# Kernel optimization log

Hardware: AMD Instinct MI355X
Metric: run time of the kernel (lower is better)

Reference implementation:

```python
import jax, jax.numpy as jnp
import numpy as np

N_HEADS = 16


def setup_inputs() -> dict:
    key = jax.random.key(0)
    k1, k2, k3 = jax.random.split(key, 3)
    B, S, D = 2, 2048, 1024
    x = jax.random.normal(k1, (B, S, D), dtype=jnp.float32)
    # causal mask: 1 = keep, 0 = masked (module does masked_fill(mask == 0, -inf))
    mask = jnp.broadcast_to(jnp.tril(jnp.ones((S, S), dtype=jnp.int32)), (B, S, S))
    # torch Linear(bias=False) weights, stored transposed so y = x @ W
    w_qkv = jax.random.normal(k2, (D, 3 * D), dtype=jnp.float32) * (1.0 / np.sqrt(D))
    w_out = jax.random.normal(k3, (D, D), dtype=jnp.float32) * (1.0 / np.sqrt(D))
    return {"x": x, "mask": mask, "w_qkv": w_qkv, "w_out": w_out}


def reference(x, mask, w_qkv, w_out):
    B, S, D = x.shape
    H = N_HEADS
    dh = D // H
    scale = 1.0 / np.sqrt(dh)

    qkv = x @ w_qkv                                   # [B,S,3D]
    qkv = qkv.reshape(B, S, 3, H, dh)
    qkv = jnp.transpose(qkv, (2, 0, 3, 1, 4))         # [3,B,H,S,dh]
    q, k, v = qkv[0], qkv[1], qkv[2]

    scores = jnp.einsum("bhqd,bhkd->bhqk", q, k) * scale   # [B,H,S,S]
    scores = jnp.where(mask[:, None, :, :] == 0, -jnp.inf, scores)
    attn = jax.nn.softmax(scores, axis=-1)            # dropout = identity (eval)

    out = jnp.einsum("bhqk,bhkd->bhqd", attn, v)      # [B,H,S,dh]
    out = jnp.transpose(out, (0, 2, 1, 3)).reshape(B, S, D)
    return out @ w_out
```

## Files before the change

kernel.cpp:

```cpp
#include <hip/hip_runtime.h>

typedef unsigned short u16;
typedef unsigned int u32;
typedef u16 u16x8 __attribute__((ext_vector_type(8)));
typedef u16 u16x4 __attribute__((ext_vector_type(4)));
typedef u32 u32x4 __attribute__((ext_vector_type(4)));
typedef __bf16 bf16x8 __attribute__((ext_vector_type(8)));
typedef float f32x4 __attribute__((ext_vector_type(4)));
typedef float f32x16 __attribute__((ext_vector_type(16)));


static __device__ __forceinline__ u16 bf16_rn(float f) {
    union { float f; u32 u; } a; a.f = f;
    u32 u = a.u;
    return (u16)((u + 0x7FFFu + ((u >> 16) & 1u)) >> 16);
}

static __device__ __forceinline__ bf16x8 as_bf(u16x8 v) {
    return __builtin_bit_cast(bf16x8, v);
}

static __device__ __forceinline__ u32 cvt_pk_bf16(float lo, float hi) {
    u32 r;
    asm("v_cvt_pk_bf16_f32 %0, %1, %2" : "=v"(r) : "v"(lo), "v"(hi));
    return r;
}

static __device__ __forceinline__ void glds16(const u16* g, u16* lds) {
    __builtin_amdgcn_global_load_lds(
        (const __attribute__((address_space(1))) void*)g,
        (__attribute__((address_space(3))) void*)lds, 16, 0, 0);
}


__global__ void k_prep(const float* __restrict__ x, u16* __restrict__ xb,
                       const float* __restrict__ w_qkv, u16* __restrict__ wqkvT,
                       const float* __restrict__ w_out, u16* __restrict__ woutT) {
    __shared__ float t[32][33];
    const int bid = blockIdx.x, tid = threadIdx.x;
    if (bid < 2048) {
        const int i = bid * 256 + tid;
        const float4* s = (const float4*)x + (size_t)i * 2;
        float4 a = s[0], b = s[1];
        u16x8 v;
        v[0] = bf16_rn(a.x); v[1] = bf16_rn(a.y); v[2] = bf16_rn(a.z); v[3] = bf16_rn(a.w);
        v[4] = bf16_rn(b.x); v[5] = bf16_rn(b.y); v[6] = bf16_rn(b.z); v[7] = bf16_rn(b.w);
        *(u16x8*)(xb + (size_t)i * 8) = v;
        return;
    }
    const float* src; u16* dst; int R, C, bxi, byi;
    if (bid < 5120) {
        const int tb = bid - 2048;
        src = w_qkv; dst = wqkvT; R = 1024; C = 3072;
        bxi = tb % 96; byi = tb / 96;
    } else {
        const int tb = bid - 5120;
        src = w_out; dst = woutT; R = 1024; C = 1024;
        bxi = tb % 32; byi = tb / 32;
    }
    const int tx = tid & 31, ty = tid >> 5;
    const int bx = bxi * 32, by = byi * 32;
#pragma unroll
    for (int j = 0; j < 32; j += 8)
        t[ty + j][tx] = src[(size_t)(by + ty + j) * C + bx + tx];
    __syncthreads();
#pragma unroll
    for (int j = 0; j < 32; j += 8)
        dst[(size_t)(bx + ty + j) * R + by + tx] = bf16_rn(t[tx][ty + j]);
}


template <int MODE>
__launch_bounds__(256, 2)
__global__ void k_gemm(const u16* __restrict__ A, const u16* __restrict__ Bt,
                       void* __restrict__ outp, int M, int N, int K) {
    __shared__ __align__(16) u16 As[2][128 * 32];
    __shared__ __align__(16) u16 Bs[2][128 * 32];
    const int tid = threadIdx.x;
    const int l = tid & 63, wv = tid >> 6;
    const int wr = wv >> 1, wc = wv & 1;
    const int l15 = l & 15, lg = l >> 4;
    const int m0 = blockIdx.y * 128, n0 = blockIdx.x * 128;
    const int NT = K >> 5;

    const f32x4 fzero = {0.f, 0.f, 0.f, 0.f};
    f32x4 acc[4][4];
#pragma unroll
    for (int m = 0; m < 4; m++)
#pragma unroll
        for (int n = 0; n < 4; n++) acc[m][n] = fzero;

    const int grow0 = wv * 32 + (l >> 2);
    const int gcol = (l & 3) * 8;

    auto stage = [&](int buf, int kt) {
        const size_t ko = (size_t)kt * 32 + gcol;
        glds16(A  + (size_t)(m0 + grow0) * K + ko,      &As[buf][wv * 1024]);
        glds16(A  + (size_t)(m0 + grow0 + 16) * K + ko, &As[buf][wv * 1024 + 512]);
        glds16(Bt + (size_t)(n0 + grow0) * K + ko,      &Bs[buf][wv * 1024]);
        glds16(Bt + (size_t)(n0 + grow0 + 16) * K + ko, &Bs[buf][wv * 1024 + 512]);
    };

    stage(0, 0);
    int cur = 0;
    for (int kt = 0; kt < NT; ++kt) {
        if (kt + 1 < NT) {
            stage(cur ^ 1, kt + 1);
            asm volatile("s_waitcnt vmcnt(4)" ::: "memory");
        } else {
            asm volatile("s_waitcnt vmcnt(0)" ::: "memory");
        }
        __builtin_amdgcn_s_barrier();
        u16x8 af[4], bfv[4];
#pragma unroll
        for (int m = 0; m < 4; m++)
            af[m] = *(const u16x8*)(&As[cur][(wr * 64 + m * 16 + l15) * 32 + lg * 8]);
#pragma unroll
        for (int n = 0; n < 4; n++)
            bfv[n] = *(const u16x8*)(&Bs[cur][(wc * 64 + n * 16 + l15) * 32 + lg * 8]);
#pragma unroll
        for (int m = 0; m < 4; m++)
#pragma unroll
            for (int n = 0; n < 4; n++)
                acc[m][n] = __builtin_amdgcn_mfma_f32_16x16x32_bf16(
                    as_bf(af[m]), as_bf(bfv[n]), acc[m][n], 0, 0, 0);
        __builtin_amdgcn_s_barrier();
        cur ^= 1;
    }

    if (MODE == 0) {
        u16* qkv = (u16*)outp;
#pragma unroll
        for (int m = 0; m < 4; m++) {
            const int rb = m0 + wr * 64 + m * 16 + lg * 4;
#pragma unroll
            for (int n = 0; n < 4; n++) {
                const int c = n0 + wc * 64 + n * 16;
                const int t = c >> 10, h = (c >> 6) & 15, d0 = (c & 63) + l15;
                const float scl = (t == 0) ? 0.18033688011112042f : 1.0f;
#pragma unroll
                for (int i = 0; i < 4; i++) {
                    const int r = rb + i;
                    const int b = r >> 11, s = r & 2047;
                    qkv[((((size_t)t * 2 + b) * 16 + h) * 2048 + s) * 64 + d0] =
                        bf16_rn(acc[m][n][i] * scl);
                }
            }
        }
    } else {
        float* O = (float*)outp;
#pragma unroll
        for (int m = 0; m < 4; m++) {
            const int rb = m0 + wr * 64 + m * 16 + lg * 4;
#pragma unroll
            for (int n = 0; n < 4; n++) {
                const int c = n0 + wc * 64 + n * 16 + l15;
#pragma unroll
                for (int i = 0; i < 4; i++)
                    O[(size_t)(rb + i) * N + c] = acc[m][n][i];
            }
        }
    }
}


__launch_bounds__(256, 2)
__global__ void k_attn(const u16* __restrict__ qkv, u16* __restrict__ ab) {
    __shared__ __align__(16) char arena[4][9216];
    __shared__ float MLs[4][64];
    const int tid = threadIdx.x, l = tid & 63, wv = tid >> 6;
    const int q = l & 31, h = l >> 5;
    const int bid = blockIdx.x;
    const int bh = bid & 31;
    const int pp = bid >> 5;
    const int b = bh >> 4, hd = bh & 15;
    const size_t plane = (size_t)2048 * 64;
    const u16* Qg = qkv + ((size_t)(0 + b) * 16 + hd) * plane;
    const u16* Kg = qkv + ((size_t)(2 + b) * 16 + hd) * plane;
    const u16* Vg = qkv + ((size_t)(4 + b) * 16 + hd) * plane;
    u16* VT = (u16*)arena[wv];

    const int g = l & 7, qd = l >> 3;
    const u16* Kbase = Kg + (size_t)q * 64 + 8 * h;
    const u16* Vbase = Vg + (size_t)(8 * qd) * 64 + 8 * g;
    const int Fq0 = 8 * (q >> 3) + ((q & 7) ^ ((q >> 3) & 7));
    const int d1 = q + 32;
    const int Fq1 = 8 * (d1 >> 3) + ((d1 & 7) ^ ((d1 >> 3) & 7));
    const u16* vr0 = VT + Fq0 * 72 + 8 * h;
    const u16* vr1 = VT + Fq1 * 72 + 8 * h;
    const float FIXM = 12.0f;

    for (int ph = 0; ph < 2; ++ph) {
        const int qt = ph ? 63 - pp : pp;
        const int q0 = qt * 32, qg = q0 + q;
        const int n64 = (qt >> 1) + 1;

        u16x8 qf[4];
#pragma unroll
        for (int s = 0; s < 4; ++s)
            qf[s] = *(const u16x8*)(Qg + (size_t)(q0 + q) * 64 + s * 16 + 8 * h);

        f32x16 oacc0 = 0, oacc1 = 0;
        float l_run = 0.f;

        u16x8 vK[8], vV[8];
        if (wv < n64) {
#pragma unroll
            for (int s = 0; s < 4; ++s) {
                vK[s]     = *(const u16x8*)(Kbase + (size_t)(wv * 64) * 64 + s * 16);
                vK[4 + s] = *(const u16x8*)(Kbase + (size_t)(wv * 64 + 32) * 64 + s * 16);
            }
#pragma unroll
            for (int j = 0; j < 8; ++j)
                vV[j] = *(const u16x8*)(Vbase + (size_t)(wv * 64 + j) * 64);
        }

        for (int t = wv; t < n64; t += 4) {
            const int kv0 = t * 64;
            f32x16 sa = 0, sb = 0;
            __builtin_amdgcn_s_setprio(1);
#pragma unroll
            for (int s = 0; s < 4; ++s)
                sa = __builtin_amdgcn_mfma_f32_32x32x16_bf16(as_bf(vK[s]), as_bf(qf[s]), sa, 0, 0, 0);
#pragma unroll
            for (int s = 0; s < 4; ++s)
                sb = __builtin_amdgcn_mfma_f32_32x32x16_bf16(as_bf(vK[4 + s]), as_bf(qf[s]), sb, 0, 0, 0);
            __builtin_amdgcn_s_setprio(0);
            {
                u32x4 vw[8];
#pragma unroll
                for (int r = 0; r < 8; ++r) vw[r] = __builtin_bit_cast(u32x4, vV[r]);
#pragma unroll
                for (int j = 0; j < 8; ++j) {
                    const u32 selc = (j & 1) ? 0x07060302u : 0x05040100u;
                    const int jr = j >> 1;
                    u32x4 cw;
#pragma unroll
                    for (int w = 0; w < 4; ++w)
                        cw[w] = __builtin_amdgcn_perm(vw[2 * w + 1][jr], vw[2 * w][jr], selc);
                    *(u32x4*)(VT + (size_t)(8 * g + (j ^ g)) * 72 + 8 * qd) = cw;
                }
            }
            if (t + 4 < n64) {
#pragma unroll
                for (int s = 0; s < 4; ++s) {
                    vK[s]     = *(const u16x8*)(Kbase + (size_t)((t + 4) * 64) * 64 + s * 16);
                    vK[4 + s] = *(const u16x8*)(Kbase + (size_t)((t + 4) * 64 + 32) * 64 + s * 16);
                }
#pragma unroll
                for (int j = 0; j < 8; ++j)
                    vV[j] = *(const u16x8*)(Vbase + (size_t)((t + 4) * 64 + j) * 64);
            }
            if (t == n64 - 1) {
#pragma unroll
                for (int r = 0; r < 16; ++r) {
                    const int kg = kv0 + (r & 3) + 8 * (r >> 2) + 4 * h;
                    if (kg > qg) sa[r] = -__builtin_inff();
                    if (kg + 32 > qg) sb[r] = -__builtin_inff();
                }
            }
#pragma unroll
            for (int r = 0; r < 16; ++r) sa[r] = exp2f(sa[r] - FIXM);
#pragma unroll
            for (int r = 0; r < 16; ++r) sb[r] = exp2f(sb[r] - FIXM);
            float ts[8];
#pragma unroll
            for (int i = 0; i < 8; ++i)
                ts[i] = (sa[i] + sa[i + 8]) + (sb[i] + sb[i + 8]);
#pragma unroll
            for (int i = 0; i < 4; ++i) ts[i] += ts[i + 4];
            l_run += (ts[0] + ts[2]) + (ts[1] + ts[3]);
            u32 pk[16];
#pragma unroll
            for (int i = 0; i < 8; ++i) pk[i]     = cvt_pk_bf16(sa[2 * i], sa[2 * i + 1]);
#pragma unroll
            for (int i = 0; i < 8; ++i) pk[8 + i] = cvt_pk_bf16(sb[2 * i], sb[2 * i + 1]);
#pragma unroll
            for (int ks = 0; ks < 4; ++ks) {
                const int base = (ks >> 1) * 8 + 4 * (ks & 1);
                u32 w0 = pk[base],     w1 = pk[base + 1];
                u32 w2 = pk[base + 2], w3 = pk[base + 3];
                asm("v_permlane32_swap_b32 %0, %1" : "+v"(w0), "+v"(w2));
                asm("v_permlane32_swap_b32 %0, %1" : "+v"(w1), "+v"(w3));
                const u16x8 pb = __builtin_bit_cast(u16x8, (u32x4){w0, w1, w2, w3});
                const u16x8 va0 = *(const u16x8*)(vr0 + ks * 16);
                const u16x8 va1 = *(const u16x8*)(vr1 + ks * 16);
                __builtin_amdgcn_s_setprio(1);
                oacc0 = __builtin_amdgcn_mfma_f32_32x32x16_bf16(as_bf(va0), as_bf(pb), oacc0, 0, 0, 0);
                oacc1 = __builtin_amdgcn_mfma_f32_32x32x16_bf16(as_bf(va1), as_bf(pb), oacc1, 0, 0, 0);
                __builtin_amdgcn_s_setprio(0);
            }
        }
        asm volatile("" ::: "memory");
        float* Op = (float*)arena[wv];
#pragma unroll
        for (int r = 0; r < 16; ++r) {
            const int dr = (r & 3) + 8 * (r >> 2) + 4 * h;
            Op[q * 64 + ((dr + 2 * q) & 63)]      = oacc0[r];
            Op[q * 64 + ((dr + 32 + 2 * q) & 63)] = oacc1[r];
        }
        MLs[wv][l] = l_run;
        __syncthreads();
        const int tq = tid >> 3, dblk = (tid & 7) * 8;
        float L = 0.f;
#pragma unroll
        for (int w = 0; w < 4; ++w) L += MLs[w][tq] + MLs[w][32 + tq];
        const float inv = 1.f / L;
        u16x8 outv;
#pragma unroll
        for (int j = 0; j < 8; ++j) {
            const int d = dblk + j;
            float acc = 0.f;
#pragma unroll
            for (int w = 0; w < 4; ++w)
                acc += ((const float*)arena[w])[tq * 64 + ((d + 2 * tq) & 63)];
            outv[j] = bf16_rn(acc * inv);
        }
        *(u16x8*)(ab + (size_t)(b * 2048 + q0 + tq) * 1024 + hd * 64 + dblk) = outv;
        __syncthreads();
    }
}


extern "C" void kernel_launch(void* const* d_in, const int* in_sizes, int n_in,
                              void* d_out, int out_size, void* d_ws, size_t ws_size,
                              hipStream_t stream) {
    const float* x     = (const float*)d_in[0];
    const float* w_qkv = (const float*)d_in[2];
    const float* w_out = (const float*)d_in[3];
    float* out = (float*)d_out;
    u16* ws = (u16*)d_ws;

    u16* xb    = ws;
    u16* wqkvT = ws + 4194304;
    u16* woutT = ws + 7340032;
    u16* qkvb  = ws + 8388608;
    u16* abuf  = ws;

    k_prep<<<6144, 256, 0, stream>>>(x, xb, w_qkv, wqkvT, w_out, woutT);
    k_gemm<0><<<dim3(24, 32), 256, 0, stream>>>(xb, wqkvT, qkvb, 4096, 3072, 1024);
    k_attn<<<1024, 256, 0, stream>>>(qkvb, abuf);
    k_gemm<1><<<dim3(8, 32), 256, 0, stream>>>(abuf, woutT, out, 4096, 1024, 1024);
}
```

Baseline: 122.9 us.

## Split 64-key tile into two sequential 32-key halves and raise occupancy

The attention inner loop now computes scores, softmax exponentials and the PV MFMAs for the first 32 keys before computing the second 32-key score block. This shortens live ranges: only one 16-float score accumulator is held at a time, and the K prefetch for each half is issued as soon as that half's registers are free. Launch bounds are raised from 2 to 3 blocks per SIMD-unit target so the compiler limits VGPRs and more waves can hide latency. The risk is spilling under the tighter register budget and less interleaving of independent MFMA chains within a wave.

After: 179.5 us. 46.1% more time.

```diff
diff --git a/kernel.cpp b/kernel.cpp
--- a/kernel.cpp
+++ b/kernel.cpp
@@ -164,7 +164,7 @@
 }
 
 
-__launch_bounds__(256, 2)
+__launch_bounds__(256, 3)
 __global__ void k_attn(const u16* __restrict__ qkv, u16* __restrict__ ab) {
     __shared__ __align__(16) char arena[4][9216];
     __shared__ float MLs[4][64];
@@ -217,14 +217,13 @@
 
         for (int t = wv; t < n64; t += 4) {
             const int kv0 = t * 64;
-            f32x16 sa = 0, sb = 0;
+            const bool diag = (t == n64 - 1);
+            const bool more = (t + 4 < n64);
+            f32x16 sa = 0;
             __builtin_amdgcn_s_setprio(1);
 #pragma unroll
             for (int s = 0; s < 4; ++s)
                 sa = __builtin_amdgcn_mfma_f32_32x32x16_bf16(as_bf(vK[s]), as_bf(qf[s]), sa, 0, 0, 0);
-#pragma unroll
-            for (int s = 0; s < 4; ++s)
-                sb = __builtin_amdgcn_mfma_f32_32x32x16_bf16(as_bf(vK[4 + s]), as_bf(qf[s]), sb, 0, 0, 0);
             __builtin_amdgcn_s_setprio(0);
             {
                 u32x4 vw[8];
@@ -241,45 +240,37 @@
                     *(u32x4*)(VT + (size_t)(8 * g + (j ^ g)) * 72 + 8 * qd) = cw;
                 }
             }
-            if (t + 4 < n64) {
-#pragma unroll
-                for (int s = 0; s < 4; ++s) {
-                    vK[s]     = *(const u16x8*)(Kbase + (size_t)((t + 4) * 64) * 64 + s * 16);
-                    vK[4 + s] = *(const u16x8*)(Kbase + (size_t)((t + 4) * 64 + 32) * 64 + s * 16);
-                }
+            if (more) {
 #pragma unroll
                 for (int j = 0; j < 8; ++j)
                     vV[j] = *(const u16x8*)(Vbase + (size_t)((t + 4) * 64 + j) * 64);
-            }
-            if (t == n64 - 1) {
+#pragma unroll
+                for (int s = 0; s < 4; ++s)
+                    vK[s] = *(const u16x8*)(Kbase + (size_t)((t + 4) * 64) * 64 + s * 16);
+            }
+            if (diag) {
 #pragma unroll
                 for (int r = 0; r < 16; ++r) {
                     const int kg = kv0 + (r & 3) + 8 * (r >> 2) + 4 * h;
                     if (kg > qg) sa[r] = -__builtin_inff();
-                    if (kg + 32 > qg) sb[r] = -__builtin_inff();
                 }
             }
 #pragma unroll
             for (int r = 0; r < 16; ++r) sa[r] = exp2f(sa[r] - FIXM);
-#pragma unroll
-            for (int r = 0; r < 16; ++r) sb[r] = exp2f(sb[r] - FIXM);
-            float ts[8];
-#pragma unroll
-            for (int i = 0; i < 8; ++i)
-                ts[i] = (sa[i] + sa[i + 8]) + (sb[i] + sb[i + 8]);
-#pragma unroll
-            for (int i = 0; i < 4; ++i) ts[i] += ts[i + 4];
-            l_run += (ts[0] + ts[2]) + (ts[1] + ts[3]);
-            u32 pk[16];
-#pragma unroll
-            for (int i = 0; i < 8; ++i) pk[i]     = cvt_pk_bf16(sa[2 * i], sa[2 * i + 1]);
-#pragma unroll
-            for (int i = 0; i < 8; ++i) pk[8 + i] = cvt_pk_bf16(sb[2 * i], sb[2 * i + 1]);
-#pragma unroll
-            for (int ks = 0; ks < 4; ++ks) {
-                const int base = (ks >> 1) * 8 + 4 * (ks & 1);
-                u32 w0 = pk[base],     w1 = pk[base + 1];
-                u32 w2 = pk[base + 2], w3 = pk[base + 3];
+            {
+                float ts[4];
+#pragma unroll
+                for (int i = 0; i < 4; ++i)
+                    ts[i] = (sa[i] + sa[i + 4]) + (sa[i + 8] + sa[i + 12]);
+                l_run += (ts[0] + ts[2]) + (ts[1] + ts[3]);
+            }
+            u32 pka[8];
+#pragma unroll
+            for (int i = 0; i < 8; ++i) pka[i] = cvt_pk_bf16(sa[2 * i], sa[2 * i + 1]);
+#pragma unroll
+            for (int ks = 0; ks < 2; ++ks) {
+                u32 w0 = pka[4 * ks],     w1 = pka[4 * ks + 1];
+                u32 w2 = pka[4 * ks + 2], w3 = pka[4 * ks + 3];
                 asm("v_permlane32_swap_b32 %0, %1" : "+v"(w0), "+v"(w2));
                 asm("v_permlane32_swap_b32 %0, %1" : "+v"(w1), "+v"(w3));
                 const u16x8 pb = __builtin_bit_cast(u16x8, (u32x4){w0, w1, w2, w3});
@@ -290,6 +281,50 @@
                 oacc1 = __builtin_amdgcn_mfma_f32_32x32x16_bf16(as_bf(va1), as_bf(pb), oacc1, 0, 0, 0);
                 __builtin_amdgcn_s_setprio(0);
             }
+            f32x16 sb = 0;
+            __builtin_amdgcn_s_setprio(1);
+#pragma unroll
+            for (int s = 0; s < 4; ++s)
+                sb = __builtin_amdgcn_mfma_f32_32x32x16_bf16(as_bf(vK[4 + s]), as_bf(qf[s]), sb, 0, 0, 0);
+            __builtin_amdgcn_s_setprio(0);
+            if (more) {
+#pragma unroll
+                for (int s = 0; s < 4; ++s)
+                    vK[4 + s] = *(const u16x8*)(Kbase + (size_t)((t + 4) * 64 + 32) * 64 + s * 16);
+            }
+            if (diag) {
+#pragma unroll
+                for (int r = 0; r < 16; ++r) {
+                    const int kg = kv0 + 32 + (r & 3) + 8 * (r >> 2) + 4 * h;
+                    if (kg > qg) sb[r] = -__builtin_inff();
+                }
+            }
+#pragma unroll
+            for (int r = 0; r < 16; ++r) sb[r] = exp2f(sb[r] - FIXM);
+            {
+                float ts[4];
+#pragma unroll
+                for (int i = 0; i < 4; ++i)
+                    ts[i] = (sb[i] + sb[i + 4]) + (sb[i + 8] + sb[i + 12]);
+                l_run += (ts[0] + ts[2]) + (ts[1] + ts[3]);
+            }
+            u32 pkb[8];
+#pragma unroll
+            for (int i = 0; i < 8; ++i) pkb[i] = cvt_pk_bf16(sb[2 * i], sb[2 * i + 1]);
+#pragma unroll
+            for (int ks = 0; ks < 2; ++ks) {
+                u32 w0 = pkb[4 * ks],     w1 = pkb[4 * ks + 1];
+                u32 w2 = pkb[4 * ks + 2], w3 = pkb[4 * ks + 3];
+                asm("v_permlane32_swap_b32 %0, %1" : "+v"(w0), "+v"(w2));
+                asm("v_permlane32_swap_b32 %0, %1" : "+v"(w1), "+v"(w3));
+                const u16x8 pb = __builtin_bit_cast(u16x8, (u32x4){w0, w1, w2, w3});
+                const u16x8 va0 = *(const u16x8*)(vr0 + (2 + ks) * 16);
+                const u16x8 va1 = *(const u16x8*)(vr1 + (2 + ks) * 16);
+                __builtin_amdgcn_s_setprio(1);
+                oacc0 = __builtin_amdgcn_mfma_f32_32x32x16_bf16(as_bf(va0), as_bf(pb), oacc0, 0, 0, 0);
+                oacc1 = __builtin_amdgcn_mfma_f32_32x32x16_bf16(as_bf(va1), as_bf(pb), oacc1, 0, 0, 0);
+                __builtin_amdgcn_s_setprio(0);
+            }
         }
         asm volatile("" ::: "memory");
         float* Op = (float*)arena[wv];
```
